# Kernel optimization log

Hardware: AMD Instinct MI355X
Metric: run time of the kernel (lower is better)

Reference implementation:

```python
import jax, jax.numpy as jnp
import numpy as np

B, CIN, CMID, H, W = 2, 64, 128, 96, 96
KWIN = 7          # attention_window
DIL = 1           # attention_stride (dilation)
GROUPS = 16
EPS = 1e-5
SCALE = float(np.sqrt(CMID))  # torch: math.sqrt(intermediate_channels), multiplies logits (NATTEN semantics)


def group_norm(x, w, b):
    # x: [B,C,H,W], 16 groups, per-channel affine
    Bx, C, Hx, Wx = x.shape
    xg = x.reshape(Bx, GROUPS, C // GROUPS, Hx, Wx)
    mu = xg.mean(axis=(2, 3, 4), keepdims=True)
    var = xg.var(axis=(2, 3, 4), keepdims=True)
    xg = (xg - mu) * jax.lax.rsqrt(var + EPS)
    return xg.reshape(Bx, C, Hx, Wx) * w[None, :, None, None] + b[None, :, None, None]


def neighborhood_attention_2d(q, k, v, ksz, scale):
    # q,k,v: [B,H,W,C]; NATTEN-style neighborhood attention, dilation=1.
    Hh, Ww = q.shape[1], q.shape[2]
    half = ksz // 2
    # window start per query, clipped so every query sees exactly ksz keys per axis
    si = jnp.clip(jnp.arange(Hh) - half, 0, Hh - ksz)          # [H]
    sj = jnp.clip(jnp.arange(Ww) - half, 0, Ww - ksz)          # [W]
    idx_i = si[:, None] + jnp.arange(ksz)[None, :]             # [H,k]
    idx_j = sj[:, None] + jnp.arange(ksz)[None, :]             # [W,k]
    kw = k[:, idx_i][:, :, :, idx_j]                           # [B,H,k,W,k,C]
    vw = v[:, idx_i][:, :, :, idx_j]                           # [B,H,k,W,k,C]
    logits = jnp.einsum('bijc,biajkc->bijak', q, kw) * scale   # [B,H,W,k,k]
    Bq = logits.shape[0]
    attn = jax.nn.softmax(logits.reshape(Bq, Hh, Ww, ksz * ksz), axis=-1)
    attn = attn.reshape(Bq, Hh, Ww, ksz, ksz)
    return jnp.einsum('bijak,biajkc->bijc', attn, vw)          # [B,H,W,C]


def setup_inputs() -> dict:
    key = jax.random.key(0)
    ks = jax.random.split(key, 6)

    def wtz(k, shape, fan):
        return (jax.random.normal(k, shape, jnp.float32) / np.sqrt(fan)).astype(jnp.float32)

    return {
        'x': jax.random.normal(ks[0], (B, CIN, H, W), jnp.float32),
        'gn_w': jnp.ones((CIN,), jnp.float32),
        'gn_b': jnp.zeros((CIN,), jnp.float32),
        'conv_w': wtz(ks[1], (CMID, CIN, 3, 3), CIN * 9),
        'conv_b': jnp.zeros((CMID,), jnp.float32),
        'q_w': wtz(ks[2], (CMID, CMID), CMID),
        'q_b': jnp.zeros((CMID,), jnp.float32),
        'k_w': wtz(ks[3], (CMID, CMID), CMID),
        'k_b': jnp.zeros((CMID,), jnp.float32),
        'v_w': wtz(ks[4], (CMID, CMID), CMID),
        'v_b': jnp.zeros((CMID,), jnp.float32),
    }


def reference(x, gn_w, gn_b, conv_w, conv_b, q_w, q_b, k_w, k_b, v_w, v_b):
    xn = group_norm(x, gn_w, gn_b)
    # 3x3 conv, padding=1 + exact GELU (torch nn.GELU default)
    f = jax.lax.conv_general_dilated(
        xn, conv_w, window_strides=(1, 1), padding=((1, 1), (1, 1)),
        dimension_numbers=('NCHW', 'OIHW', 'NCHW')) + conv_b[None, :, None, None]
    f = jax.nn.gelu(f, approximate=False)
    # 1x1 QKV convs
    q = jnp.einsum('bchw,oc->bohw', f, q_w) + q_b[None, :, None, None]
    k = jnp.einsum('bchw,oc->bohw', f, k_w) + k_b[None, :, None, None]
    v = jnp.einsum('bchw,oc->bohw', f, v_w) + v_b[None, :, None, None]
    # to NHWC (singleton head dim squeezed)
    qh = q.transpose(0, 2, 3, 1)
    kh = k.transpose(0, 2, 3, 1)
    vh = v.transpose(0, 2, 3, 1)
    ksz = min(KWIN, f.shape[2], f.shape[3])
    ksz -= 1 if ksz % 2 == 0 else 0
    out = neighborhood_attention_2d(qh, kh, vh, ksz, SCALE)
    return out.transpose(0, 3, 1, 2)  # back to NCHW
```

## Files before the change

kernel.cpp:

```cpp
#include <hip/hip_runtime.h>
#include <math.h>

#define Hh 96
#define Ww 96
#define HW 9216
#define CIN 64
#define CMID 128
#define NAT_SCALE 11.313708498984761f

typedef __attribute__((ext_vector_type(4))) float f32x4;
typedef __attribute__((ext_vector_type(8))) short short8;

__device__ __forceinline__ unsigned short f2bf(float x) {
    union { float f; unsigned u; } v; v.f = x;
    unsigned r = v.u + 0x7FFF + ((v.u >> 16) & 1);
    return (unsigned short)(r >> 16);
}
__device__ __forceinline__ float bf2f(unsigned short h) {
    union { unsigned u; float f; } v; v.u = (unsigned)h << 16;
    return v.f;
}

__global__ __launch_bounds__(256) void gn_partial_kernel(const float* __restrict__ x,
    float2* __restrict__ partials)
{
    int blk = blockIdx.x;
    int tid = threadIdx.x;
    size_t base = (size_t)(blk >> 4) * 36864 + (size_t)(blk & 15) * 2304;
    float s = 0.f, s2 = 0.f;
    #pragma unroll
    for (int i = 0; i < 9; ++i) {
        float v = x[base + i * 256 + tid];
        s += v; s2 += v * v;
    }
    #pragma unroll
    for (int d = 1; d < 64; d <<= 1) {
        s  += __shfl_xor(s, d);
        s2 += __shfl_xor(s2, d);
    }
    __shared__ float as[4], as2[4];
    int wid = tid >> 6, lane = tid & 63;
    if (lane == 0) { as[wid] = s; as2[wid] = s2; }
    __syncthreads();
    if (tid == 0) {
        float2 r = { as[0]+as[1]+as[2]+as[3], as2[0]+as2[1]+as2[2]+as2[3] };
        partials[blk] = r;
    }
}

__global__ __launch_bounds__(256) void border_kernel(
    unsigned short* __restrict__ xh, unsigned short* __restrict__ xl)
{
    int t = blockIdx.x * 256 + threadIdx.x;
    if (t >= 6208) return;
    int b = t / 3104, r = t - b * 3104;
    int pos = r >> 3, gc = r & 7;
    int y, xx;
    if (pos < 98)      { y = 0;          xx = pos; }
    else if (pos < 196){ y = 97;         xx = pos - 98; }
    else if (pos < 292){ y = pos - 195;  xx = 0; }
    else               { y = pos - 291;  xx = 97; }
    size_t off = ((size_t)(b * 98 + y) * 98 + xx) * 64 + gc * 8;
    short8 z = {0,0,0,0,0,0,0,0};
    *(short8*)(xh + off) = z;
    *(short8*)(xl + off) = z;
}

__global__ __launch_bounds__(256) void gnapply_kernel(const float* __restrict__ x,
    const float2* __restrict__ partials,
    const float* __restrict__ gw, const float* __restrict__ gb,
    unsigned short* __restrict__ xh, unsigned short* __restrict__ xl)
{
    __shared__ float tin[64 * 25];
    __shared__ float sgld[32];
    int blk = blockIdx.x;
    int b = blk / 384, r1 = blk - b * 384;
    int y = r1 >> 2, q = r1 & 3;
    int tid = threadIdx.x;

    if (tid < 256) {
        float2 pv = partials[b * 256 + tid];
        float s = pv.x, s2 = pv.y;
        #pragma unroll
        for (int d = 1; d < 16; d <<= 1) {
            s  += __shfl_xor(s, d);
            s2 += __shfl_xor(s2, d);
        }
        if ((tid & 15) == 0) {
            const float invN = 1.f / 36864.f;
            float mean = s * invN;
            float var  = s2 * invN - mean * mean;
            sgld[(tid >> 4) * 2]     = mean;
            sgld[(tid >> 4) * 2 + 1] = rsqrtf(var + 1e-5f);
        }
    }
    #pragma unroll
    for (int i = 0; i < 6; ++i) {
        int idx = i * 256 + tid;
        int c = idx / 24, xx = idx - c * 24;
        tin[c * 25 + xx] = x[((size_t)(b * CIN + c)) * HW + y * Ww + q * 24 + xx];
    }
    __syncthreads();
    #pragma unroll
    for (int i = 0; i < 6; ++i) {
        int idx = i * 256 + tid;
        int xx = idx >> 6, c = idx & 63;
        float v = tin[c * 25 + xx];
        float val = (v - sgld[(c >> 2) * 2]) * sgld[(c >> 2) * 2 + 1] * gw[c] + gb[c];
        unsigned short hi = f2bf(val);
        unsigned short lo = f2bf(val - bf2f(hi));
        size_t dst = ((size_t)(b * 98 + y + 1) * 98 + q * 24 + xx + 1) * 64 + c;
        xh[dst] = hi; xl[dst] = lo;
    }
}

__global__ __launch_bounds__(256) void repack_kernel(const float* __restrict__ cw,
    const float* __restrict__ qw, const float* __restrict__ kw_,
    const float* __restrict__ vw,
    unsigned short* __restrict__ wch, unsigned short* __restrict__ wcl,
    unsigned short* __restrict__ wqh, unsigned short* __restrict__ wql)
{
    int t = blockIdx.x * 256 + threadIdx.x;
    if (t < 73728) {
        int e = t & 7, l = (t >> 3) & 63, fr = (t >> 9) & 1;
        int ocg = (t >> 10) & 3, s2 = t >> 12;
        int s = s2 >> 1, ch = s2 & 1;
        int oc = ocg * 32 + fr * 16 + (l & 15);
        int c  = ch * 32 + (l >> 4) * 8 + e;
        float v = cw[oc * 576 + c * 9 + s];
        unsigned short hi = f2bf(v);
        wch[t] = hi; wcl[t] = f2bf(v - bf2f(hi));
    } else {
        int t2 = t - 73728;
        int e = t2 & 7, l = (t2 >> 3) & 63, fr = (t2 >> 9) & 1;
        int ocg = (t2 >> 10) & 3, kc2 = (t2 >> 12) & 3, m = t2 >> 14;
        int oc = ocg * 32 + fr * 16 + (l & 15);
        int c  = kc2 * 32 + (l >> 4) * 8 + e;
        const float* W = (m == 0) ? qw : (m == 1) ? kw_ : vw;
        float v = W[oc * 128 + c];
        unsigned short hi = f2bf(v);
        wqh[t2] = hi; wql[t2] = f2bf(v - bf2f(hi));
    }
}

#define MFMA3(ACC, AH, AL, BH, BL) \
    ACC = __builtin_amdgcn_mfma_f32_16x16x32_bf16(AL, BH, ACC, 0, 0, 0); \
    ACC = __builtin_amdgcn_mfma_f32_16x16x32_bf16(AH, BL, ACC, 0, 0, 0); \
    ACC = __builtin_amdgcn_mfma_f32_16x16x32_bf16(AH, BH, ACC, 0, 0, 0);

__global__ __launch_bounds__(512) void convqkv_kernel(
    const unsigned short* __restrict__ xh, const unsigned short* __restrict__ xl,
    const unsigned short* __restrict__ wch, const unsigned short* __restrict__ wcl,
    const float* __restrict__ cb,
    const unsigned short* __restrict__ wqh, const unsigned short* __restrict__ wql,
    const float* __restrict__ qbias, const float* __restrict__ kbias,
    const float* __restrict__ vbias,
    float* __restrict__ qo, float* __restrict__ ko, float* __restrict__ vo)
{
    __shared__ __align__(16) short ph_s[3840];
    __shared__ __align__(16) short pl_s[3840];
    __shared__ __align__(16) short fh_s[4096];
    __shared__ __align__(16) short fl_s[4096];
    int bid = blockIdx.x;
    int swz = (bid & 7) * 72 + (bid >> 3);
    int b = swz / 288, rem = swz - b * 288;
    int ty = rem / 12, tx = rem - ty * 12;
    int y0 = ty * 4, x0 = tx * 8;
    int tid = threadIdx.x;

    if (tid < 480) {
        int g = tid;
        int row = g / 80, r2 = g - row * 80;
        int col = r2 >> 3, gc = r2 & 7;
        size_t srcoff = ((size_t)(b * 98 + y0 + row) * 98 + x0 + col) * 64 + gc * 8;
        int dst = ((row * 10 + col) << 6) + ((gc ^ (col & 7)) << 3);
        *(short8*)&ph_s[dst] = *(const short8*)(xh + srcoff);
        *(short8*)&pl_s[dst] = *(const short8*)(xl + srcoff);
    }
    __syncthreads();

    int wid = tid >> 6, l = tid & 63;
    int posg = wid >> 2, ocg = wid & 3;
    int l15 = l & 15, l4 = l >> 4;
    int oc0 = ocg * 32;
    int p0 = posg * 16 + l15;
    int r0 = p0 >> 3, xc = p0 & 7;

    f32x4 c00 = {0.f,0.f,0.f,0.f}, c01 = {0.f,0.f,0.f,0.f};

    #pragma unroll 3
    for (int s = 0; s < 9; ++s) {
        int dy = s / 3, dx = s - dy * 3;
        int colA = xc + dx, cswz = (colA & 7) << 3;
        #pragma unroll
        for (int ch = 0; ch < 2; ++ch) {
            int gr = (ch * 4 + l4) << 3;
            int ai = (((r0 + dy) * 10 + colA) << 6) + (gr ^ cswz);
            short8 ah = *(const short8*)&ph_s[ai];
            short8 al = *(const short8*)&pl_s[ai];
            int s2 = s * 2 + ch;
            int wb = ((s2 * 4 + ocg) * 2) * 512 + l * 8;
            short8 b0h = *(const short8*)(wch + wb);
            short8 b0l = *(const short8*)(wcl + wb);
            short8 b1h = *(const short8*)(wch + wb + 512);
            short8 b1l = *(const short8*)(wcl + wb + 512);
            MFMA3(c00, ah, al, b0h, b0l)
            MFMA3(c01, ah, al, b1h, b1l)
        }
    }

    float bias0 = cb[oc0 + l15], bias1 = cb[oc0 + 16 + l15];
    #pragma unroll
    for (int nf = 0; nf < 2; ++nf) {
        f32x4 a = nf == 0 ? c00 : c01;
        float bs = nf == 0 ? bias0 : bias1;
        int oc = oc0 + nf * 16 + l15;
        #pragma unroll
        for (int rr = 0; rr < 4; ++rr) {
            int p = posg * 16 + l4 * 4 + rr;
            float v = a[rr] + bs;
            float g = 0.5f * v * (1.f + erff(v * 0.70710678118654752f));
            unsigned short hi = f2bf(g);
            unsigned short lo = f2bf(g - bf2f(hi));
            int di = p * 128 + ((((oc >> 3) ^ (p & 7)) << 3) | (oc & 7));
            fh_s[di] = (short)hi;
            fl_s[di] = (short)lo;
        }
    }
    __syncthreads();

    short8 aqh[4], aql[4];
    #pragma unroll
    for (int kc2 = 0; kc2 < 4; ++kc2) {
        int gr2 = (kc2 * 4 + l4) << 3;
        int i0 = p0 * 128 + (gr2 ^ ((p0 & 7) << 3));
        aqh[kc2] = *(const short8*)&fh_s[i0];
        aql[kc2] = *(const short8*)&fl_s[i0];
    }

    #pragma unroll 1
    for (int m = 0; m < 3; ++m) {
        const float* Bi = (m == 0) ? qbias : (m == 1) ? kbias : vbias;
        float* Om = (m == 0) ? qo : (m == 1) ? ko : vo;
        f32x4 d0 = {0.f,0.f,0.f,0.f}, d1 = {0.f,0.f,0.f,0.f};
        #pragma unroll
        for (int kc2 = 0; kc2 < 4; ++kc2) {
            int wb = (((m * 4 + kc2) * 4 + ocg) * 2) * 512 + l * 8;
            short8 b0h = *(const short8*)(wqh + wb);
            short8 b0l = *(const short8*)(wql + wb);
            short8 b1h = *(const short8*)(wqh + wb + 512);
            short8 b1l = *(const short8*)(wql + wb + 512);
            MFMA3(d0, aqh[kc2], aql[kc2], b0h, b0l)
            MFMA3(d1, aqh[kc2], aql[kc2], b1h, b1l)
        }
        float bm0 = Bi[oc0 + l15], bm1 = Bi[oc0 + 16 + l15];
        #pragma unroll
        for (int nf = 0; nf < 2; ++nf) {
            f32x4 a = nf == 0 ? d0 : d1;
            float bs = nf == 0 ? bm0 : bm1;
            int oc = oc0 + nf * 16 + l15;
            #pragma unroll
            for (int rr = 0; rr < 4; ++rr) {
                int p = posg * 16 + l4 * 4 + rr;
                int yy = y0 + (p >> 3), xx = x0 + (p & 7);
                Om[((size_t)(b * HW + yy * Ww + xx)) * CMID + oc] = a[rr] + bs;
            }
        }
    }
}

__global__ __launch_bounds__(256) void nat_kernel(const float* __restrict__ q,
    const float* __restrict__ k, const float* __restrict__ v,
    float* __restrict__ out)
{
    int bid = blockIdx.x;
    int swz = (bid & 7) * 144 + (bid >> 3);
    int tid = threadIdx.x;
    int wid = tid >> 6, lane = tid & 63;
    int g = __builtin_amdgcn_readfirstlane(swz * 4 + wid);
    int b = g / 2304, rem = g - b * 2304;
    int ti = rem / 48, tj = rem - ti * 48;
    int i0 = ti * 2, j0 = tj * 2;

    int si0 = i0 - 3; si0 = si0 < 0 ? 0 : (si0 > 89 ? 89 : si0);
    int si1 = i0 - 2; si1 = si1 < 0 ? 0 : (si1 > 89 ? 89 : si1);
    int sj0 = j0 - 3; sj0 = sj0 < 0 ? 0 : (sj0 > 89 ? 89 : sj0);
    int sj1 = j0 - 2; sj1 = sj1 < 0 ? 0 : (sj1 > 89 ? 89 : sj1);
    int ui = si0 > 88 ? 88 : si0;
    int uj = sj0 > 88 ? 88 : sj0;
    int oi0 = si0 - ui, oi1 = si1 - ui, oj0 = sj0 - uj, oj1 = sj1 - uj;
    int base2 = b * HW + ui * Ww + uj;

    int wr = lane >> 3, wc = lane & 7;

    const float4* kp  = (const float4*)(k + (size_t)(base2 + wr * Ww + wc) * CMID);
    const float4* qp0 = (const float4*)(q + (size_t)(b * HW + i0 * Ww + j0) * CMID);
    const float4* qp2 = (const float4*)(q + (size_t)(b * HW + (i0 + 1) * Ww + j0) * CMID);
    float a0 = 0.f, a1 = 0.f, a2 = 0.f, a3 = 0.f;
    #pragma unroll
    for (int c = 0; c < 32; ++c) {
        float4 kv = kp[c];
        float4 q0 = qp0[c], q1 = qp0[c + 32], q2 = qp2[c], q3 = qp2[c + 32];
        a0 = fmaf(q0.x, kv.x, a0); a0 = fmaf(q0.y, kv.y, a0);
        a0 = fmaf(q0.z, kv.z, a0); a0 = fmaf(q0.w, kv.w, a0);
        a1 = fmaf(q1.x, kv.x, a1); a1 = fmaf(q1.y, kv.y, a1);
        a1 = fmaf(q1.z, kv.z, a1); a1 = fmaf(q1.w, kv.w, a1);
        a2 = fmaf(q2.x, kv.x, a2); a2 = fmaf(q2.y, kv.y, a2);
        a2 = fmaf(q2.z, kv.z, a2); a2 = fmaf(q2.w, kv.w, a2);
        a3 = fmaf(q3.x, kv.x, a3); a3 = fmaf(q3.y, kv.y, a3);
        a3 = fmaf(q3.z, kv.z, a3); a3 = fmaf(q3.w, kv.w, a3);
    }

    float l0 = ((unsigned)(wr - oi0) <= 6u && (unsigned)(wc - oj0) <= 6u) ? a0 * NAT_SCALE : -INFINITY;
    float l1 = ((unsigned)(wr - oi0) <= 6u && (unsigned)(wc - oj1) <= 6u) ? a1 * NAT_SCALE : -INFINITY;
    float l2 = ((unsigned)(wr - oi1) <= 6u && (unsigned)(wc - oj0) <= 6u) ? a2 * NAT_SCALE : -INFINITY;
    float l3 = ((unsigned)(wr - oi1) <= 6u && (unsigned)(wc - oj1) <= 6u) ? a3 * NAT_SCALE : -INFINITY;
    float m0 = l0, m1 = l1, m2 = l2, m3 = l3;
    #pragma unroll
    for (int d = 1; d < 64; d <<= 1) {
        m0 = fmaxf(m0, __shfl_xor(m0, d)); m1 = fmaxf(m1, __shfl_xor(m1, d));
        m2 = fmaxf(m2, __shfl_xor(m2, d)); m3 = fmaxf(m3, __shfl_xor(m3, d));
    }
    float e0 = __expf(l0 - m0), e1 = __expf(l1 - m1);
    float e2 = __expf(l2 - m2), e3 = __expf(l3 - m3);
    float s0 = e0, s1 = e1, s2 = e2, s3 = e3;
    #pragma unroll
    for (int d = 1; d < 64; d <<= 1) {
        s0 += __shfl_xor(s0, d); s1 += __shfl_xor(s1, d);
        s2 += __shfl_xor(s2, d); s3 += __shfl_xor(s3, d);
    }
    float w0 = e0 / s0, w1 = e1 / s1, w2 = e2 / s2, w3 = e3 / s3;

    const float2* vbase = (const float2*)(v + (size_t)base2 * CMID);
    float2 o0 = {0.f, 0.f}, o1 = {0.f, 0.f}, o2 = {0.f, 0.f}, o3 = {0.f, 0.f};
    #pragma unroll
    for (int w = 0; w < 64; ++w) {
        int off = ((w >> 3) * Ww + (w & 7)) * 64;
        float2 vv = vbase[off + lane];
        float b0 = __shfl(w0, w), b1 = __shfl(w1, w);
        float b2 = __shfl(w2, w), b3 = __shfl(w3, w);
        o0.x = fmaf(b0, vv.x, o0.x); o0.y = fmaf(b0, vv.y, o0.y);
        o1.x = fmaf(b1, vv.x, o1.x); o1.y = fmaf(b1, vv.y, o1.y);
        o2.x = fmaf(b2, vv.x, o2.x); o2.y = fmaf(b2, vv.y, o2.y);
        o3.x = fmaf(b3, vv.x, o3.x); o3.y = fmaf(b3, vv.y, o3.y);
    }

    size_t ob = ((size_t)(b * CMID + 2 * lane)) * HW + i0 * Ww + j0;
    float2 r0 = {o0.x, o1.x}, r1 = {o0.y, o1.y};
    float2 r2 = {o2.x, o3.x}, r3 = {o2.y, o3.y};
    *(float2*)(out + ob)           = r0;
    *(float2*)(out + ob + HW)      = r1;
    *(float2*)(out + ob + Ww)      = r2;
    *(float2*)(out + ob + HW + Ww) = r3;
}

extern "C" void kernel_launch(void* const* d_in, const int* in_sizes, int n_in,
                              void* d_out, int out_size, void* d_ws, size_t ws_size,
                              hipStream_t stream) {
    const float* x      = (const float*)d_in[0];
    const float* gn_w   = (const float*)d_in[1];
    const float* gn_b   = (const float*)d_in[2];
    const float* conv_w = (const float*)d_in[3];
    const float* conv_b = (const float*)d_in[4];
    const float* q_w    = (const float*)d_in[5];
    const float* q_b    = (const float*)d_in[6];
    const float* k_w    = (const float*)d_in[7];
    const float* k_b    = (const float*)d_in[8];
    const float* v_w    = (const float*)d_in[9];
    const float* v_b    = (const float*)d_in[10];

    const size_t XNP = (size_t)2 * 98 * 98 * 64;
    float* ws    = (float*)d_ws;
    float2* partials = (float2*)ws;
    float* qb_   = ws + 1024;
    float* kb_   = qb_ + (size_t)2 * CMID * HW;
    float* vb_   = kb_ + (size_t)2 * CMID * HW;
    unsigned short* xnh = (unsigned short*)(vb_ + (size_t)2 * CMID * HW);
    unsigned short* xnl = xnh + XNP;
    unsigned short* wch = xnl + XNP;
    unsigned short* wcl = wch + 73728;
    unsigned short* wqh = wcl + 73728;
    unsigned short* wql = wqh + 49152;

    gn_partial_kernel<<<512, 256, 0, stream>>>(x, partials);
    border_kernel<<<25, 256, 0, stream>>>(xnh, xnl);
    repack_kernel<<<480, 256, 0, stream>>>(conv_w, q_w, k_w, v_w,
                                           wch, wcl, wqh, wql);
    gnapply_kernel<<<768, 256, 0, stream>>>(x, partials, gn_w, gn_b, xnh, xnl);
    convqkv_kernel<<<576, 512, 0, stream>>>(xnh, xnl, wch, wcl, conv_b,
                                            wqh, wql, q_b, k_b, v_b,
                                            qb_, kb_, vb_);
    nat_kernel<<<1152, 256, 0, stream>>>(qb_, kb_, vb_, (float*)d_out);
}
```

Measured before the change: 85.76 us.

## Merge prep kernels, double per-wave tile in conv, stage K tile in LDS

```diff
diff --git a/kernel.cpp b/kernel.cpp
--- a/kernel.cpp
+++ b/kernel.cpp
@@ -21,49 +21,74 @@
     return v.f;
 }
 
-__global__ __launch_bounds__(256) void gn_partial_kernel(const float* __restrict__ x,
-    float2* __restrict__ partials)
-{
-    int blk = blockIdx.x;
-    int tid = threadIdx.x;
-    size_t base = (size_t)(blk >> 4) * 36864 + (size_t)(blk & 15) * 2304;
-    float s = 0.f, s2 = 0.f;
-    #pragma unroll
-    for (int i = 0; i < 9; ++i) {
-        float v = x[base + i * 256 + tid];
-        s += v; s2 += v * v;
-    }
-    #pragma unroll
-    for (int d = 1; d < 64; d <<= 1) {
-        s  += __shfl_xor(s, d);
-        s2 += __shfl_xor(s2, d);
-    }
-    __shared__ float as[4], as2[4];
-    int wid = tid >> 6, lane = tid & 63;
-    if (lane == 0) { as[wid] = s; as2[wid] = s2; }
-    __syncthreads();
-    if (tid == 0) {
-        float2 r = { as[0]+as[1]+as[2]+as[3], as2[0]+as2[1]+as2[2]+as2[3] };
-        partials[blk] = r;
-    }
-}
-
-__global__ __launch_bounds__(256) void border_kernel(
+__global__ __launch_bounds__(256) void prep_kernel(const float* __restrict__ x,
+    float2* __restrict__ partials,
+    const float* __restrict__ cw, const float* __restrict__ qw,
+    const float* __restrict__ kw_, const float* __restrict__ vw,
+    unsigned short* __restrict__ wch, unsigned short* __restrict__ wcl,
+    unsigned short* __restrict__ wqh, unsigned short* __restrict__ wql,
     unsigned short* __restrict__ xh, unsigned short* __restrict__ xl)
 {
-    int t = blockIdx.x * 256 + threadIdx.x;
-    if (t >= 6208) return;
-    int b = t / 3104, r = t - b * 3104;
-    int pos = r >> 3, gc = r & 7;
-    int y, xx;
-    if (pos < 98)      { y = 0;          xx = pos; }
-    else if (pos < 196){ y = 97;         xx = pos - 98; }
-    else if (pos < 292){ y = pos - 195;  xx = 0; }
-    else               { y = pos - 291;  xx = 97; }
-    size_t off = ((size_t)(b * 98 + y) * 98 + xx) * 64 + gc * 8;
-    short8 z = {0,0,0,0,0,0,0,0};
-    *(short8*)(xh + off) = z;
-    *(short8*)(xl + off) = z;
+    int bid = blockIdx.x, tid = threadIdx.x;
+    if (bid < 512) {
+        size_t base = (size_t)(bid >> 4) * 36864 + (size_t)(bid & 15) * 2304;
+        float s = 0.f, s2 = 0.f;
+        #pragma unroll
+        for (int i = 0; i < 9; ++i) {
+            float v = x[base + i * 256 + tid];
+            s += v; s2 += v * v;
+        }
+        #pragma unroll
+        for (int d = 1; d < 64; d <<= 1) {
+            s  += __shfl_xor(s, d);
+            s2 += __shfl_xor(s2, d);
+        }
+        __shared__ float as[4], as2[4];
+        int wid = tid >> 6, lane = tid & 63;
+        if (lane == 0) { as[wid] = s; as2[wid] = s2; }
+        __syncthreads();
+        if (tid == 0) {
+            float2 r = { as[0]+as[1]+as[2]+as[3], as2[0]+as2[1]+as2[2]+as2[3] };
+            partials[bid] = r;
+        }
+    } else if (bid < 992) {
+        int t = (bid - 512) * 256 + tid;
+        if (t < 73728) {
+            int e = t & 7, l = (t >> 3) & 63, fr = (t >> 9) & 1;
+            int ocg = (t >> 10) & 3, s2 = t >> 12;
+            int s = s2 >> 1, ch = s2 & 1;
+            int oc = ocg * 32 + fr * 16 + (l & 15);
+            int c  = ch * 32 + (l >> 4) * 8 + e;
+            float v = cw[oc * 576 + c * 9 + s];
+            unsigned short hi = f2bf(v);
+            wch[t] = hi; wcl[t] = f2bf(v - bf2f(hi));
+        } else {
+            int t2 = t - 73728;
+            int e = t2 & 7, l = (t2 >> 3) & 63, fr = (t2 >> 9) & 1;
+            int ocg = (t2 >> 10) & 3, kc2 = (t2 >> 12) & 3, m = t2 >> 14;
+            int oc = ocg * 32 + fr * 16 + (l & 15);
+            int c  = kc2 * 32 + (l >> 4) * 8 + e;
+            const float* W = (m == 0) ? qw : (m == 1) ? kw_ : vw;
+            float v = W[oc * 128 + c];
+            unsigned short hi = f2bf(v);
+            wqh[t2] = hi; wql[t2] = f2bf(v - bf2f(hi));
+        }
+    } else {
+        int t = (bid - 992) * 256 + tid;
+        if (t < 6208) {
+            int b = t / 3104, r = t - b * 3104;
+            int pos = r >> 3, gc = r & 7;
+            int y, xx;
+            if (pos < 98)      { y = 0;          xx = pos; }
+            else if (pos < 196){ y = 97;         xx = pos - 98; }
+            else if (pos < 292){ y = pos - 195;  xx = 0; }
+            else               { y = pos - 291;  xx = 97; }
+            size_t off = ((size_t)(b * 98 + y) * 98 + xx) * 64 + gc * 8;
+            short8 z = {0,0,0,0,0,0,0,0};
+            *(short8*)(xh + off) = z;
+            *(short8*)(xl + off) = z;
+        }
+    }
 }
 
 __global__ __launch_bounds__(256) void gnapply_kernel(const float* __restrict__ x,
@@ -78,7 +103,7 @@
     int y = r1 >> 2, q = r1 & 3;
     int tid = threadIdx.x;
 
-    if (tid < 256) {
+    {
         float2 pv = partials[b * 256 + tid];
         float s = pv.x, s2 = pv.y;
         #pragma unroll
@@ -114,41 +139,12 @@
     }
 }
 
-__global__ __launch_bounds__(256) void repack_kernel(const float* __restrict__ cw,
-    const float* __restrict__ qw, const float* __restrict__ kw_,
-    const float* __restrict__ vw,
-    unsigned short* __restrict__ wch, unsigned short* __restrict__ wcl,
-    unsigned short* __restrict__ wqh, unsigned short* __restrict__ wql)
-{
-    int t = blockIdx.x * 256 + threadIdx.x;
-    if (t < 73728) {
-        int e = t & 7, l = (t >> 3) & 63, fr = (t >> 9) & 1;
-        int ocg = (t >> 10) & 3, s2 = t >> 12;
-        int s = s2 >> 1, ch = s2 & 1;
-        int oc = ocg * 32 + fr * 16 + (l & 15);
-        int c  = ch * 32 + (l >> 4) * 8 + e;
-        float v = cw[oc * 576 + c * 9 + s];
-        unsigned short hi = f2bf(v);
-        wch[t] = hi; wcl[t] = f2bf(v - bf2f(hi));
-    } else {
-        int t2 = t - 73728;
-        int e = t2 & 7, l = (t2 >> 3) & 63, fr = (t2 >> 9) & 1;
-        int ocg = (t2 >> 10) & 3, kc2 = (t2 >> 12) & 3, m = t2 >> 14;
-        int oc = ocg * 32 + fr * 16 + (l & 15);
-        int c  = kc2 * 32 + (l >> 4) * 8 + e;
-        const float* W = (m == 0) ? qw : (m == 1) ? kw_ : vw;
-        float v = W[oc * 128 + c];
-        unsigned short hi = f2bf(v);
-        wqh[t2] = hi; wql[t2] = f2bf(v - bf2f(hi));
-    }
-}
-
 #define MFMA3(ACC, AH, AL, BH, BL) \
     ACC = __builtin_amdgcn_mfma_f32_16x16x32_bf16(AL, BH, ACC, 0, 0, 0); \
     ACC = __builtin_amdgcn_mfma_f32_16x16x32_bf16(AH, BL, ACC, 0, 0, 0); \
     ACC = __builtin_amdgcn_mfma_f32_16x16x32_bf16(AH, BH, ACC, 0, 0, 0);
 
-__global__ __launch_bounds__(512) void convqkv_kernel(
+__global__ __launch_bounds__(256) void convqkv_kernel(
     const unsigned short* __restrict__ xh, const unsigned short* __restrict__ xl,
     const unsigned short* __restrict__ wch, const unsigned short* __restrict__ wcl,
     const float* __restrict__ cb,
@@ -168,8 +164,7 @@
     int y0 = ty * 4, x0 = tx * 8;
     int tid = threadIdx.x;
 
-    if (tid < 480) {
-        int g = tid;
+    for (int g = tid; g < 480; g += 256) {
         int row = g / 80, r2 = g - row * 80;
         int col = r2 >> 3, gc = r2 & 7;
         size_t srcoff = ((size_t)(b * 98 + y0 + row) * 98 + x0 + col) * 64 + gc * 8;
@@ -179,14 +174,14 @@
     }
     __syncthreads();
 
-    int wid = tid >> 6, l = tid & 63;
-    int posg = wid >> 2, ocg = wid & 3;
+    int ocg = tid >> 6, l = tid & 63;
     int l15 = l & 15, l4 = l >> 4;
     int oc0 = ocg * 32;
-    int p0 = posg * 16 + l15;
+    int p0 = l15, p1 = 16 + l15;
     int r0 = p0 >> 3, xc = p0 & 7;
 
     f32x4 c00 = {0.f,0.f,0.f,0.f}, c01 = {0.f,0.f,0.f,0.f};
+    f32x4 c10 = {0.f,0.f,0.f,0.f}, c11 = {0.f,0.f,0.f,0.f};
 
     #pragma unroll 3
     for (int s = 0; s < 9; ++s) {
@@ -195,75 +190,88 @@
         #pragma unroll
         for (int ch = 0; ch < 2; ++ch) {
             int gr = (ch * 4 + l4) << 3;
-            int ai = (((r0 + dy) * 10 + colA) << 6) + (gr ^ cswz);
-            short8 ah = *(const short8*)&ph_s[ai];
-            short8 al = *(const short8*)&pl_s[ai];
+            int ai0 = (((r0 + dy) * 10 + colA) << 6) + (gr ^ cswz);
+            int ai1 = (((r0 + 2 + dy) * 10 + colA) << 6) + (gr ^ cswz);
+            short8 a0h = *(const short8*)&ph_s[ai0];
+            short8 a0l = *(const short8*)&pl_s[ai0];
+            short8 a1h = *(const short8*)&ph_s[ai1];
+            short8 a1l = *(const short8*)&pl_s[ai1];
             int s2 = s * 2 + ch;
             int wb = ((s2 * 4 + ocg) * 2) * 512 + l * 8;
             short8 b0h = *(const short8*)(wch + wb);
             short8 b0l = *(const short8*)(wcl + wb);
             short8 b1h = *(const short8*)(wch + wb + 512);
             short8 b1l = *(const short8*)(wcl + wb + 512);
-            MFMA3(c00, ah, al, b0h, b0l)
-            MFMA3(c01, ah, al, b1h, b1l)
+            MFMA3(c00, a0h, a0l, b0h, b0l)
+            MFMA3(c01, a0h, a0l, b1h, b1l)
+            MFMA3(c10, a1h, a1l, b0h, b0l)
+            MFMA3(c11, a1h, a1l, b1h, b1l)
         }
     }
 
     float bias0 = cb[oc0 + l15], bias1 = cb[oc0 + 16 + l15];
     #pragma unroll
-    for (int nf = 0; nf < 2; ++nf) {
-        f32x4 a = nf == 0 ? c00 : c01;
-        float bs = nf == 0 ? bias0 : bias1;
-        int oc = oc0 + nf * 16 + l15;
-        #pragma unroll
-        for (int rr = 0; rr < 4; ++rr) {
-            int p = posg * 16 + l4 * 4 + rr;
-            float v = a[rr] + bs;
-            float g = 0.5f * v * (1.f + erff(v * 0.70710678118654752f));
-            unsigned short hi = f2bf(g);
-            unsigned short lo = f2bf(g - bf2f(hi));
-            int di = p * 128 + ((((oc >> 3) ^ (p & 7)) << 3) | (oc & 7));
-            fh_s[di] = (short)hi;
-            fl_s[di] = (short)lo;
+    for (int mf = 0; mf < 2; ++mf) {
+        #pragma unroll
+        for (int nf = 0; nf < 2; ++nf) {
+            f32x4 a = (mf == 0) ? (nf == 0 ? c00 : c01) : (nf == 0 ? c10 : c11);
+            float bs = nf == 0 ? bias0 : bias1;
+            int oc = oc0 + nf * 16 + l15;
+            #pragma unroll
+            for (int rr = 0; rr < 4; ++rr) {
+                int p = mf * 16 + l4 * 4 + rr;
+                float v = a[rr] + bs;
+                float g = 0.5f * v * (1.f + erff(v * 0.70710678118654752f));
+                unsigned short hi = f2bf(g);
+                unsigned short lo = f2bf(g - bf2f(hi));
+                int di = p * 128 + ((((oc >> 3) ^ (p & 7)) << 3) | (oc & 7));
+                fh_s[di] = (short)hi;
+                fl_s[di] = (short)lo;
+            }
         }
     }
     __syncthreads();
 
-    short8 aqh[4], aql[4];
-    #pragma unroll
-    for (int kc2 = 0; kc2 < 4; ++kc2) {
-        int gr2 = (kc2 * 4 + l4) << 3;
-        int i0 = p0 * 128 + (gr2 ^ ((p0 & 7) << 3));
-        aqh[kc2] = *(const short8*)&fh_s[i0];
-        aql[kc2] = *(const short8*)&fl_s[i0];
-    }
-
+    int sw0 = (p0 & 7) << 3, sw1 = (p1 & 7) << 3;
     #pragma unroll 1
     for (int m = 0; m < 3; ++m) {
         const float* Bi = (m == 0) ? qbias : (m == 1) ? kbias : vbias;
         float* Om = (m == 0) ? qo : (m == 1) ? ko : vo;
-        f32x4 d0 = {0.f,0.f,0.f,0.f}, d1 = {0.f,0.f,0.f,0.f};
+        f32x4 d00 = {0.f,0.f,0.f,0.f}, d01 = {0.f,0.f,0.f,0.f};
+        f32x4 d10 = {0.f,0.f,0.f,0.f}, d11 = {0.f,0.f,0.f,0.f};
         #pragma unroll
         for (int kc2 = 0; kc2 < 4; ++kc2) {
+            int gr2 = (kc2 * 4 + l4) << 3;
+            int i0 = p0 * 128 + (gr2 ^ sw0);
+            int i1 = p1 * 128 + (gr2 ^ sw1);
+            short8 ah0 = *(const short8*)&fh_s[i0];
+            short8 al0 = *(const short8*)&fl_s[i0];
+            short8 ah1 = *(const short8*)&fh_s[i1];
+            short8 al1 = *(const short8*)&fl_s[i1];
             int wb = (((m * 4 + kc2) * 4 + ocg) * 2) * 512 + l * 8;
             short8 b0h = *(const short8*)(wqh + wb);
             short8 b0l = *(const short8*)(wql + wb);
             short8 b1h = *(const short8*)(wqh + wb + 512);
             short8 b1l = *(const short8*)(wql + wb + 512);
-            MFMA3(d0, aqh[kc2], aql[kc2], b0h, b0l)
-            MFMA3(d1, aqh[kc2], aql[kc2], b1h, b1l)
+            MFMA3(d00, ah0, al0, b0h, b0l)
+            MFMA3(d01, ah0, al0, b1h, b1l)
+            MFMA3(d10, ah1, al1, b0h, b0l)
+            MFMA3(d11, ah1, al1, b1h, b1l)
         }
         float bm0 = Bi[oc0 + l15], bm1 = Bi[oc0 + 16 + l15];
         #pragma unroll
-        for (int nf = 0; nf < 2; ++nf) {
-            f32x4 a = nf == 0 ? d0 : d1;
-            float bs = nf == 0 ? bm0 : bm1;
-            int oc = oc0 + nf * 16 + l15;
+        for (int mf = 0; mf < 2; ++mf) {
             #pragma unroll
-            for (int rr = 0; rr < 4; ++rr) {
-                int p = posg * 16 + l4 * 4 + rr;
-                int yy = y0 + (p >> 3), xx = x0 + (p & 7);
-                Om[((size_t)(b * HW + yy * Ww + xx)) * CMID + oc] = a[rr] + bs;
+            for (int nf = 0; nf < 2; ++nf) {
+                f32x4 a = (mf == 0) ? (nf == 0 ? d00 : d01) : (nf == 0 ? d10 : d11);
+                float bs = nf == 0 ? bm0 : bm1;
+                int oc = oc0 + nf * 16 + l15;
+                #pragma unroll
+                for (int rr = 0; rr < 4; ++rr) {
+                    int p = mf * 16 + l4 * 4 + rr;
+                    int yy = y0 + (p >> 3), xx = x0 + (p & 7);
+                    Om[((size_t)(b * HW + yy * Ww + xx)) * CMID + oc] = a[rr] + bs;
+                }
             }
         }
     }
@@ -273,34 +281,53 @@
     const float* __restrict__ k, const float* __restrict__ v,
     float* __restrict__ out)
 {
+    __shared__ __align__(16) float Kl[12800];
     int bid = blockIdx.x;
     int swz = (bid & 7) * 144 + (bid >> 3);
+    int b = swz / 576, rem = swz - b * 576;
+    int ti = rem / 24, tj = rem - ti * 24;
+    int i0 = ti * 4, j0 = tj * 4;
+    int ui = i0 - 3; ui = ui < 0 ? 0 : (ui > 86 ? 86 : ui);
+    int uj = j0 - 3; uj = uj < 0 ? 0 : (uj > 86 ? 86 : uj);
     int tid = threadIdx.x;
+
+    const float4* ksrc = (const float4*)k;
+    float4* Kl4 = (float4*)Kl;
+    #pragma unroll
+    for (int it = 0; it < 13; ++it) {
+        int idx = it * 256 + tid;
+        if (idx < 3200) {
+            int row = idx >> 5, c4 = idx & 31;
+            int ur = row / 10, uc = row - ur * 10;
+            size_t gp = ((size_t)(b * HW + (ui + ur) * Ww + (uj + uc))) * 32 + c4;
+            Kl4[row * 32 + (c4 ^ (row & 7))] = ksrc[gp];
+        }
+    }
+    __syncthreads();
+
     int wid = tid >> 6, lane = tid & 63;
-    int g = __builtin_amdgcn_readfirstlane(swz * 4 + wid);
-    int b = g / 2304, rem = g - b * 2304;
-    int ti = rem / 48, tj = rem - ti * 48;
-    int i0 = ti * 2, j0 = tj * 2;
-
-    int si0 = i0 - 3; si0 = si0 < 0 ? 0 : (si0 > 89 ? 89 : si0);
-    int si1 = i0 - 2; si1 = si1 < 0 ? 0 : (si1 > 89 ? 89 : si1);
-    int sj0 = j0 - 3; sj0 = sj0 < 0 ? 0 : (sj0 > 89 ? 89 : sj0);
-    int sj1 = j0 - 2; sj1 = sj1 < 0 ? 0 : (sj1 > 89 ? 89 : sj1);
-    int ui = si0 > 88 ? 88 : si0;
-    int uj = sj0 > 88 ? 88 : sj0;
-    int oi0 = si0 - ui, oi1 = si1 - ui, oj0 = sj0 - uj, oj1 = sj1 - uj;
-    int base2 = b * HW + ui * Ww + uj;
+    int gy = wid >> 1, gx = wid & 1;
+    int iq0 = i0 + 2 * gy, jq0 = j0 + 2 * gx;
+
+    int si0 = iq0 - 3; si0 = si0 < 0 ? 0 : (si0 > 89 ? 89 : si0);
+    int si1 = iq0 - 2; si1 = si1 < 0 ? 0 : (si1 > 89 ? 89 : si1);
+    int sj0 = jq0 - 3; sj0 = sj0 < 0 ? 0 : (sj0 > 89 ? 89 : sj0);
+    int sj1 = jq0 - 2; sj1 = sj1 < 0 ? 0 : (sj1 > 89 ? 89 : sj1);
+    int gsi = si0 > 88 ? 88 : si0;
+    int gsj = sj0 > 88 ? 88 : sj0;
+    int oi0 = si0 - gsi, oi1 = si1 - gsi, oj0 = sj0 - gsj, oj1 = sj1 - gsj;
+    int goi = gsi - ui, goj = gsj - uj;
 
     int wr = lane >> 3, wc = lane & 7;
-
-    const float4* kp  = (const float4*)(k + (size_t)(base2 + wr * Ww + wc) * CMID);
-    const float4* qp0 = (const float4*)(q + (size_t)(b * HW + i0 * Ww + j0) * CMID);
-    const float4* qp2 = (const float4*)(q + (size_t)(b * HW + (i0 + 1) * Ww + j0) * CMID);
+    int R = (goi + wr) * 10 + (goj + wc);
+    int Rs = R * 32, Rx = R & 7;
+
+    const float4* qp0 = (const float4*)(q + (size_t)(b * HW + iq0 * Ww + jq0) * CMID);
     float a0 = 0.f, a1 = 0.f, a2 = 0.f, a3 = 0.f;
-    #pragma unroll
+    #pragma unroll 8
     for (int c = 0; c < 32; ++c) {
-        float4 kv = kp[c];
-        float4 q0 = qp0[c], q1 = qp0[c + 32], q2 = qp2[c], q3 = qp2[c + 32];
+        float4 kv = Kl4[Rs + (c ^ Rx)];
+        float4 q0 = qp0[c], q1 = qp0[c + 32], q2 = qp0[c + 3072], q3 = qp0[c + 3104];
         a0 = fmaf(q0.x, kv.x, a0); a0 = fmaf(q0.y, kv.y, a0);
         a0 = fmaf(q0.z, kv.z, a0); a0 = fmaf(q0.w, kv.w, a0);
         a1 = fmaf(q1.x, kv.x, a1); a1 = fmaf(q1.y, kv.y, a1);
@@ -331,6 +358,7 @@
     }
     float w0 = e0 / s0, w1 = e1 / s1, w2 = e2 / s2, w3 = e3 / s3;
 
+    int base2 = b * HW + gsi * Ww + gsj;
     const float2* vbase = (const float2*)(v + (size_t)base2 * CMID);
     float2 o0 = {0.f, 0.f}, o1 = {0.f, 0.f}, o2 = {0.f, 0.f}, o3 = {0.f, 0.f};
     #pragma unroll
@@ -345,7 +373,7 @@
         o3.x = fmaf(b3, vv.x, o3.x); o3.y = fmaf(b3, vv.y, o3.y);
     }
 
-    size_t ob = ((size_t)(b * CMID + 2 * lane)) * HW + i0 * Ww + j0;
+    size_t ob = ((size_t)(b * CMID + 2 * lane)) * HW + iq0 * Ww + jq0;
     float2 r0 = {o0.x, o1.x}, r1 = {o0.y, o1.y};
     float2 r2 = {o2.x, o3.x}, r3 = {o2.y, o3.y};
     *(float2*)(out + ob)           = r0;
@@ -382,12 +410,10 @@
     unsigned short* wqh = wcl + 73728;
     unsigned short* wql = wqh + 49152;
 
-    gn_partial_kernel<<<512, 256, 0, stream>>>(x, partials);
-    border_kernel<<<25, 256, 0, stream>>>(xnh, xnl);
-    repack_kernel<<<480, 256, 0, stream>>>(conv_w, q_w, k_w, v_w,
-                                           wch, wcl, wqh, wql);
+    prep_kernel<<<1017, 256, 0, stream>>>(x, partials, conv_w, q_w, k_w, v_w,
+                                          wch, wcl, wqh, wql, xnh, xnl);
     gnapply_kernel<<<768, 256, 0, stream>>>(x, partials, gn_w, gn_b, xnh, xnl);
-    convqkv_kernel<<<576, 512, 0, stream>>>(xnh, xnl, wch, wcl, conv_b,
+    convqkv_kernel<<<576, 256, 0, stream>>>(xnh, xnl, wch, wcl, conv_b,
                                             wqh, wql, q_b, k_b, v_b,
                                             qb_, kb_, vb_);
     nat_kernel<<<1152, 256, 0, stream>>>(qb_, kb_, vb_, (float*)d_out);
```

Result: faster. 75.81 us (-11.6%).
